# Kernel tuning notes

Measured on AMD Instinct MI355X. Metric: run time of the kernel, lower is better.

Reference implementation:

```python
import jax, jax.numpy as jnp
import numpy as np

DIM = 128
GROUPS = [1, 2, 2, 3]


def setup_inputs() -> dict:
    key = jax.random.key(0)
    ks = jax.random.split(key, 8)
    c = DIM
    def p(k, shape, scale=0.02):
        return jax.random.normal(k, shape, dtype=jnp.float32) * scale
    return {
        "x": jax.random.normal(ks[0], (8, c, 128, 128), dtype=jnp.float32),
        "temperature": jnp.ones((4, 1, 1), dtype=jnp.float32),
        "w_qkv": p(ks[1], (3 * c, c)),            # Conv2d(dim, 3*dim, 1), bias=False
        "w_dw": p(ks[2], (3 * c, 1, 3, 3)),        # depthwise 3x3, groups=3*dim
        "w_proj": p(ks[3], (c, c)),                # Conv2d(dim, dim, 1), bias=False
        "w_gate": p(ks[4], (c, c)),                # Intra gatingConv (Conv1d k=1)
        "b_gate": jnp.zeros((c,), jnp.float32),
        "w_down": p(ks[5], (c // 2, c)),           # Intra down
        "b_down": jnp.zeros((c // 2,), jnp.float32),
        "w_up": p(ks[6], (c, c // 2)),             # Intra up
        "b_up": jnp.zeros((c,), jnp.float32),
    }


def _group_sizes(c):
    total = sum(GROUPS)
    sizes = [int(r / total * c) for r in GROUPS]
    sizes[-1] += c - sum(sizes)
    return sizes


def _forward(x, temperature, w_qkv, w_dw, w_proj, w_gate, b_gate,
             w_down, b_down, w_up, b_up):
    b, c, h, w = x.shape
    L = h * w
    # qkv = dwconv3x3(conv1x1(x))
    qkv = jnp.einsum('bchw,oc->bohw', x, w_qkv)
    qkv = jax.lax.conv_general_dilated(
        qkv, w_dw, (1, 1), 'SAME', feature_group_count=3 * c,
        dimension_numbers=('NCHW', 'OIHW', 'NCHW'))
    q, k, v = jnp.split(qkv.reshape(b, 3 * c, L), 3, axis=1)
    # ReGroup: sort channels by mean q activation (descending), split into groups
    channel_mean = q.mean(axis=(0, 2))            # (c,)
    idx = jnp.argsort(-channel_mean)
    q, k, v = q[:, idx], k[:, idx], v[:, idx]
    sizes = _group_sizes(c)
    outs, caches, cache_means = [], [], []
    start = 0
    for i, g in enumerate(sizes):
        qg = q[:, start:start + g]
        kg = k[:, start:start + g]
        vg = v[:, start:start + g]
        start += g
        qn = qg / jnp.maximum(jnp.linalg.norm(qg, axis=-1, keepdims=True), 1e-12)
        kn = kg / jnp.maximum(jnp.linalg.norm(kg, axis=-1, keepdims=True), 1e-12)
        attn = jax.nn.softmax(
            jnp.einsum('bcl,bdl->bcd', qn, kn) * temperature[i, 0, 0], axis=-1)
        outs.append(jnp.einsum('bcd,bdl->bcl', attn, vg))   # (b, g, L)
        tc = jax.lax.stop_gradient(qn + kn)                 # detached cache
        caches.append(tc)
        # per-group mean over L, channel-tiled/padded to c (for cache update)
        gm = tc.mean(axis=-1)                               # (b, g)
        rep = max(1, c // g)
        gm = jnp.tile(gm, (1, rep))
        gm = gm[:, :c] if gm.shape[1] >= c else jnp.pad(gm, ((0, 0), (0, c - gm.shape[1])))
        cache_means.append(gm)
    out_all = jnp.concatenate(outs, axis=1)       # (b, c, L)
    tmp_caches = jnp.concatenate(caches, axis=1)  # (b, c, L)
    # CalculateCurrentLayerCache: bilinear upsample of (1,1) map == broadcast
    s = int(L ** 0.5 + 0.9999)
    acc = sum(cache_means) / float(len(cache_means))        # (b, c)
    qv_cache = jnp.broadcast_to((acc * 0.9)[:, :, None, None], (b, c, s, s))
    # Intra cache modulation: gated = gelu(conv(x1+x2)) * (x1+x2); up(down(gated))
    sxy = out_all + tmp_caches
    gating = jax.nn.gelu(jnp.einsum('bcl,oc->bol', sxy, w_gate) + b_gate[:, None],
                         approximate=False)
    gated = gating * sxy
    mod = jnp.einsum('bcl,oc->bol', gated, w_down) + b_down[:, None]
    mod = jnp.einsum('bcl,oc->bol', mod, w_up) + b_up[:, None]
    out_all = mod + out_all
    out_all = jnp.einsum('bchw,oc->bohw', out_all.reshape(b, c, h, w), w_proj)
    return out_all, qv_cache


def reference(x, temperature, w_qkv, w_dw, w_proj, w_gate, b_gate,
              w_down, b_down, w_up, b_up):
    return _forward(x, temperature, w_qkv, w_dw, w_proj, w_gate, b_gate,
                    w_down, b_down, w_up, b_up)
```

## Files before the change

### kernel.cpp

```cpp
#include <hip/hip_runtime.h>
#include <math.h>

#define B_ 8
#define C_ 128
#define O3_ 384
#define H_ 128
#define W_ 128
#define L_ 16384
#define NS_ 64
#define MAXP_ 2304

typedef float f32x4 __attribute__((ext_vector_type(4)));
typedef short bf16x8 __attribute__((ext_vector_type(8)));

static __device__ __forceinline__ ushort f2bf(float f) {
    uint u = __float_as_uint(f);
    u += 0x7fffu + ((u >> 16) & 1u);
    return (ushort)(u >> 16);
}
static __device__ __forceinline__ float bf2f(ushort h) {
    return __uint_as_float(((uint)h) << 16);
}

__global__ __launch_bounds__(256) void wsplit_k(
    const float* __restrict__ wa, const float* __restrict__ wb,
    const float* __restrict__ wc, const float* __restrict__ wd,
    short* __restrict__ ha, short* __restrict__ la,
    short* __restrict__ hb, short* __restrict__ lb,
    short* __restrict__ hc, short* __restrict__ lc,
    short* __restrict__ hd, short* __restrict__ ld)
{
    const int sel = blockIdx.y;
    const float* w = sel == 0 ? wa : (sel == 1 ? wb : (sel == 2 ? wc : wd));
    short* ph = sel == 0 ? ha : (sel == 1 ? hb : (sel == 2 ? hc : hd));
    short* pl = sel == 0 ? la : (sel == 1 ? lb : (sel == 2 ? lc : ld));
    const int n = sel == 0 ? 49152 : (sel == 1 ? 16384 : 8192);
    const int i = blockIdx.x * 256 + threadIdx.x;
    if (i < n) {
        float v = w[i];
        ushort h = f2bf(v);
        ph[i] = (short)h;
        pl[i] = (short)f2bf(v - bf2f(h));
    }
}

__global__ __launch_bounds__(256) void wsplit1_k(const float* __restrict__ w,
    short* __restrict__ ph, short* __restrict__ pl, int n)
{
    const int i = blockIdx.x * 256 + threadIdx.x;
    if (i < n) {
        float v = w[i];
        ushort h = f2bf(v);
        ph[i] = (short)h;
        pl[i] = (short)f2bf(v - bf2f(h));
    }
}

__global__ __launch_bounds__(256) void transp_k(const float* __restrict__ x,
    short* __restrict__ xhi, short* __restrict__ xlo)
{
    __shared__ float t[128][33];
    const int b = blockIdx.y;
    const int l0 = blockIdx.x * 32;
    const int tid = threadIdx.x;
    {
        const int c = tid >> 1, half = tid & 1;
        const float* src = x + ((size_t)b * C_ + c) * L_ + l0 + half * 16;
#pragma unroll
        for (int u = 0; u < 4; u++) {
            float4 v = *reinterpret_cast<const float4*>(src + u * 4);
            t[c][half * 16 + u * 4 + 0] = v.x;
            t[c][half * 16 + u * 4 + 1] = v.y;
            t[c][half * 16 + u * 4 + 2] = v.z;
            t[c][half * 16 + u * 4 + 3] = v.w;
        }
    }
    __syncthreads();
    {
        const int l = tid >> 3, strip = tid & 7;
        uint hi[8], lo[8];
#pragma unroll
        for (int i = 0; i < 8; i++) {
            float a0 = t[strip * 16 + 2 * i][l], a1 = t[strip * 16 + 2 * i + 1][l];
            ushort h0 = f2bf(a0), h1 = f2bf(a1);
            ushort g0 = f2bf(a0 - bf2f(h0)), g1 = f2bf(a1 - bf2f(h1));
            hi[i] = (uint)h0 | ((uint)h1 << 16);
            lo[i] = (uint)g0 | ((uint)g1 << 16);
        }
        size_t ob = ((size_t)b * L_ + l0 + l) * C_ + strip * 16;
        uint4* ph = reinterpret_cast<uint4*>(xhi + ob);
        uint4* pl = reinterpret_cast<uint4*>(xlo + ob);
        ph[0] = *reinterpret_cast<uint4*>(&hi[0]);
        ph[1] = *reinterpret_cast<uint4*>(&hi[4]);
        pl[0] = *reinterpret_cast<uint4*>(&lo[0]);
        pl[1] = *reinterpret_cast<uint4*>(&lo[4]);
    }
}

template<int KD, int OT, int MODE>
__global__ __launch_bounds__(256) void mgemm_k(
    const short* __restrict__ Whi, const short* __restrict__ Wlo,
    const float* __restrict__ bias,
    const short* __restrict__ Ahi, const short* __restrict__ Alo,
    const float* __restrict__ E0,
    float* __restrict__ Yf, short* __restrict__ Yhi, short* __restrict__ Ylo)
{
    constexpr int NR = OT / 32;
    constexpr int T = KD / 32;
    constexpr int BPT = (OT * 4) / 256;
    __shared__ short sAh[128][40];
    __shared__ short sAl[128][40];
    __shared__ short sBh[OT][40];
    __shared__ short sBl[OT][40];
    const int tid = threadIdx.x;
    const int lane = tid & 63;
    const int wid = tid >> 6;
    const int wr = wid >> 1, wc = wid & 1;
    const int oB = blockIdx.x * OT;
    const int lB = blockIdx.y * 128;
    const int ON = gridDim.x * OT;
    const int b = blockIdx.z;
    const int ln15 = lane & 15, lg = lane >> 4;

    const int al0 = tid >> 2, ac8 = (tid & 3) * 8;
    const size_t abase = ((size_t)b * L_ + lB + al0) * KD + ac8;

    f32x4 acc[4][NR];
#pragma unroll
    for (int m = 0; m < 4; m++)
#pragma unroll
        for (int n = 0; n < NR; n++)
#pragma unroll
            for (int r = 0; r < 4; r++) acc[m][n][r] = 0.f;

    bf16x8 pAh[2], pAl[2], pBh[BPT], pBl[BPT];

    auto ldA = [&](int t) {
#pragma unroll
        for (int p = 0; p < 2; p++) {
            size_t g = abase + (size_t)p * 64 * KD + t * 32;
            pAh[p] = *reinterpret_cast<const bf16x8*>(Ahi + g);
            pAl[p] = *reinterpret_cast<const bf16x8*>(Alo + g);
        }
    };
    auto ldB = [&](int t) {
#pragma unroll
        for (int p = 0; p < BPT; p++) {
            int idx = tid + p * 256;
            int o = idx >> 2, c8 = (idx & 3) * 8;
            size_t g = (size_t)(oB + o) * KD + t * 32 + c8;
            pBh[p] = *reinterpret_cast<const bf16x8*>(Whi + g);
            pBl[p] = *reinterpret_cast<const bf16x8*>(Wlo + g);
        }
    };
    auto stAB = [&]() {
#pragma unroll
        for (int p = 0; p < 2; p++) {
            *reinterpret_cast<bf16x8*>(&sAh[al0 + p * 64][ac8]) = pAh[p];
            *reinterpret_cast<bf16x8*>(&sAl[al0 + p * 64][ac8]) = pAl[p];
        }
#pragma unroll
        for (int p = 0; p < BPT; p++) {
            int idx = tid + p * 256;
            int o = idx >> 2, c8 = (idx & 3) * 8;
            *reinterpret_cast<bf16x8*>(&sBh[o][c8]) = pBh[p];
            *reinterpret_cast<bf16x8*>(&sBl[o][c8]) = pBl[p];
        }
    };

    ldA(0); ldB(0);
    stAB();
    __syncthreads();

    for (int t = 0; t < T; t++) {
        if (t + 1 < T) { ldA(t + 1); ldB(t + 1); }
        bf16x8 Ah[4], Al[4];
#pragma unroll
        for (int m = 0; m < 4; m++) {
            int row = wr * 64 + m * 16 + ln15;
            Ah[m] = *reinterpret_cast<const bf16x8*>(&sAh[row][lg * 8]);
            Al[m] = *reinterpret_cast<const bf16x8*>(&sAl[row][lg * 8]);
        }
#pragma unroll
        for (int n = 0; n < NR; n++) {
            int brow = wc * (OT / 2) + n * 16 + ln15;
            bf16x8 Bh = *reinterpret_cast<const bf16x8*>(&sBh[brow][lg * 8]);
            bf16x8 Bl = *reinterpret_cast<const bf16x8*>(&sBl[brow][lg * 8]);
#pragma unroll
            for (int m = 0; m < 4; m++) {
                acc[m][n] = __builtin_amdgcn_mfma_f32_16x16x32_bf16(Ah[m], Bh, acc[m][n], 0, 0, 0);
                acc[m][n] = __builtin_amdgcn_mfma_f32_16x16x32_bf16(Ah[m], Bl, acc[m][n], 0, 0, 0);
                acc[m][n] = __builtin_amdgcn_mfma_f32_16x16x32_bf16(Al[m], Bh, acc[m][n], 0, 0, 0);
            }
        }
        __syncthreads();
        if (t + 1 < T) { stAB(); __syncthreads(); }
    }

#pragma unroll
    for (int m = 0; m < 4; m++) {
        const int lg4 = lB + wr * 64 + m * 16 + lg * 4;
#pragma unroll
        for (int n = 0; n < NR; n++) {
            const int o = oB + wc * (OT / 2) + n * 16 + ln15;
            if constexpr (MODE == 4) {
                float4 r4 = {acc[m][n][0], acc[m][n][1], acc[m][n][2], acc[m][n][3]};
                *reinterpret_cast<float4*>(&Yf[((size_t)b * ON + o) * L_ + lg4]) = r4;
            } else {
                float bv = bias[o];
#pragma unroll
                for (int r = 0; r < 4; r++) {
                    size_t yi = ((size_t)b * L_ + lg4 + r) * ON + o;
                    float a = acc[m][n][r] + bv;
                    if constexpr (MODE == 1) {
                        float sxy = bf2f((ushort)Ahi[yi]) + bf2f((ushort)Alo[yi]);
                        a = 0.5f * a * (1.f + erff(a * 0.70710678118654752f)) * sxy;
                    }
                    if constexpr (MODE == 3) a += E0[yi];
                    ushort h = f2bf(a);
                    ushort g = f2bf(a - bf2f(h));
                    Yhi[yi] = (short)h;
                    Ylo[yi] = (short)g;
                }
            }
        }
    }
}

__global__ __launch_bounds__(256) void dwconv_k(const float* __restrict__ in,
    const float* __restrict__ wdw, float* __restrict__ outp,
    float* __restrict__ sumq, float* __restrict__ sumk,
    float* __restrict__ ssq, float* __restrict__ ssk)
{
    const int ch = blockIdx.x, b = blockIdx.y;
    const int tid = threadIdx.x;
    const int tx = tid & 31, band = tid >> 5;
    const int x0 = tx * 4;
    const int y0 = band * 16;
    const size_t base = ((size_t)b * O3_ + ch) * L_;
    const float* wp = wdw + ch * 9;
    float w0 = wp[0], w1 = wp[1], w2 = wp[2], w3 = wp[3], w4 = wp[4],
          w5 = wp[5], w6 = wp[6], w7 = wp[7], w8 = wp[8];

    float s1 = 0.f, s2 = 0.f;
    float b0[6], b1[6], b2[6];

    auto loadrow = [&](int gy, float* r) {
        if ((unsigned)gy < (unsigned)H_) {
            const float* rp = in + base + (size_t)gy * W_;
            float4 m = *reinterpret_cast<const float4*>(rp + x0);
            r[0] = (x0 > 0) ? rp[x0 - 1] : 0.f;
            r[1] = m.x; r[2] = m.y; r[3] = m.z; r[4] = m.w;
            r[5] = (x0 < W_ - 4) ? rp[x0 + 4] : 0.f;
        } else {
            r[0] = r[1] = r[2] = r[3] = r[4] = r[5] = 0.f;
        }
    };
    auto conv3 = [&](const float* ra, const float* rb, const float* rc, int yy) {
        float o0 = ra[0]*w0 + ra[1]*w1 + ra[2]*w2 + rb[0]*w3 + rb[1]*w4 + rb[2]*w5 + rc[0]*w6 + rc[1]*w7 + rc[2]*w8;
        float o1 = ra[1]*w0 + ra[2]*w1 + ra[3]*w2 + rb[1]*w3 + rb[2]*w4 + rb[3]*w5 + rc[1]*w6 + rc[2]*w7 + rc[3]*w8;
        float o2 = ra[2]*w0 + ra[3]*w1 + ra[4]*w2 + rb[2]*w3 + rb[3]*w4 + rb[4]*w5 + rc[2]*w6 + rc[3]*w7 + rc[4]*w8;
        float o3 = ra[3]*w0 + ra[4]*w1 + ra[5]*w2 + rb[3]*w3 + rb[4]*w4 + rb[5]*w5 + rc[3]*w6 + rc[4]*w7 + rc[5]*w8;
        float4 o4 = {o0, o1, o2, o3};
        *reinterpret_cast<float4*>(&outp[base + (size_t)(y0 + yy) * W_ + x0]) = o4;
        s1 += (o0 + o1) + (o2 + o3);
        s2 += o0*o0 + o1*o1 + o2*o2 + o3*o3;
    };

    loadrow(y0 - 1, b0);
    loadrow(y0,     b1);
#pragma unroll
    for (int y3 = 0; y3 < 15; y3 += 3) {
        loadrow(y0 + y3 + 1, b2); conv3(b0, b1, b2, y3);
        loadrow(y0 + y3 + 2, b0); conv3(b1, b2, b0, y3 + 1);
        loadrow(y0 + y3 + 3, b1); conv3(b2, b0, b1, y3 + 2);
    }
    loadrow(y0 + 16, b2); conv3(b0, b1, b2, 15);

    __shared__ float r1[256], r2[256];
    if (ch < 256) {
        r1[tid] = s1; r2[tid] = s2;
        __syncthreads();
        for (int st = 128; st > 0; st >>= 1) {
            if (tid < st) { r1[tid] += r1[tid + st]; r2[tid] += r2[tid + st]; }
            __syncthreads();
        }
        if (tid == 0) {
            if (ch < 128) { sumq[b * 128 + ch] = r1[0]; ssq[b * 128 + ch] = r2[0]; }
            else          { sumk[b * 128 + ch - 128] = r1[0]; ssk[b * 128 + ch - 128] = r2[0]; }
        }
    }
}

__global__ void combine_k(const float* __restrict__ sumq, const float* __restrict__ sumk,
    const float* __restrict__ ssq, const float* __restrict__ ssk,
    int* __restrict__ idxp, float* __restrict__ rqc, float* __restrict__ rkc,
    float* __restrict__ gm)
{
    const int t = threadIdx.x;
    __shared__ double cms[128];
    double s = 0.0;
    for (int b = 0; b < B_; b++) s += (double)sumq[b * 128 + t];
    cms[t] = s;
    float rqv[B_], rkv[B_];
    for (int b = 0; b < B_; b++) {
        rqv[b] = 1.f / fmaxf(sqrtf(ssq[b * 128 + t]), 1e-12f);
        rkv[b] = 1.f / fmaxf(sqrtf(ssk[b * 128 + t]), 1e-12f);
        rqc[b * 128 + t] = rqv[b];
        rkc[b * 128 + t] = rkv[b];
    }
    __syncthreads();
    const double mv = cms[t];
    int r = 0;
    for (int j = 0; j < 128; j++) {
        double o = cms[j];
        if (o > mv || (o == mv && j < t)) r++;
    }
    idxp[r] = t;
    for (int b = 0; b < B_; b++)
        gm[b * 128 + r] = (rqv[b] * sumq[b * 128 + t] + rkv[b] * sumk[b * 128 + t]) * (1.0f / L_);
}

template<int G>
__global__ __launch_bounds__(256) void score_k(const float* __restrict__ dw, const int* __restrict__ idxp,
    int start, int gi, float* __restrict__ spart)
{
    constexpr int TS = G / 16;
    const int split = blockIdx.x, b = blockIdx.y;
    const int tid = threadIdx.x, tx = tid & 15, ty = tid >> 4;
    __shared__ float sQ[G][66];
    __shared__ float sK[G][66];
    __shared__ int sc[G];
    if (tid < G) sc[tid] = idxp[start + tid];
    __syncthreads();

    float acc[TS][TS];
#pragma unroll
    for (int i = 0; i < TS; i++)
#pragma unroll
        for (int j = 0; j < TS; j++) acc[i][j] = 0.f;

    const int l0 = split * (L_ / NS_);
    constexpr int LPT = (G * 64) / 256;
    for (int chk = 0; chk < L_ / NS_; chk += 64) {
#pragma unroll
        for (int i = 0; i < LPT; i++) {
            int id = tid + i * 256;
            int row = id >> 6, lc = id & 63;
            size_t base = ((size_t)b * O3_ + sc[row]) * L_ + l0 + chk + lc;
            sQ[row][lc] = dw[base];
            sK[row][lc] = dw[base + (size_t)128 * L_];
        }
        __syncthreads();
#pragma unroll
        for (int kk = 0; kk < 64; kk++) {
            float qv[TS], kv[TS];
#pragma unroll
            for (int j = 0; j < TS; j++) { qv[j] = sQ[ty * TS + j][kk]; kv[j] = sK[tx * TS + j][kk]; }
#pragma unroll
            for (int i = 0; i < TS; i++)
#pragma unroll
                for (int j = 0; j < TS; j++)
                    acc[i][j] = fmaf(qv[i], kv[j], acc[i][j]);
        }
        __syncthreads();
    }
    float* op = spart + (((size_t)(b * 4 + gi)) * NS_ + split) * MAXP_;
#pragma unroll
    for (int i = 0; i < TS; i++)
#pragma unroll
        for (int j = 0; j < TS; j++)
            op[(ty * TS + i) * G + tx * TS + j] = acc[i][j];
}

__global__ __launch_bounds__(256) void softmax_k(const float* __restrict__ spart,
    const float* __restrict__ rqc, const float* __restrict__ rkc, const int* __restrict__ idxp,
    const float* __restrict__ temp, float* __restrict__ attn)
{
    const int gi = blockIdx.x, b = blockIdx.y;
    const int g = (gi == 0) ? 16 : (gi == 3 ? 48 : 32);
    const int start = (gi == 0) ? 0 : (gi == 1 ? 16 : (gi == 2 ? 48 : 80));
    __shared__ float S[MAXP_];
    __shared__ int sidx[48];
    if (threadIdx.x < g) sidx[threadIdx.x] = idxp[start + threadIdx.x];
    __syncthreads();
    const float tv = temp[gi];
    for (int p = threadIdx.x; p < g * g; p += 256) {
        float s = 0.f;
        const float* sp = spart + ((size_t)(b * 4 + gi)) * NS_ * MAXP_ + p;
        for (int k = 0; k < NS_; k++) s += sp[(size_t)k * MAXP_];
        int cc = p / g, dd = p - cc * g;
        S[p] = s * rqc[b * 128 + sidx[cc]] * rkc[b * 128 + sidx[dd]] * tv;
    }
    __syncthreads();
    const int wv = threadIdx.x >> 6, lane = threadIdx.x & 63;
    for (int r = wv; r < g; r += 4) {
        float val = (lane < g) ? S[r * g + lane] : -1e30f;
        float mx = val;
        for (int m = 32; m > 0; m >>= 1) mx = fmaxf(mx, __shfl_xor(mx, m));
        float e = (lane < g) ? expf(val - mx) : 0.f;
        float sum = e;
        for (int m = 32; m > 0; m >>= 1) sum += __shfl_xor(sum, m);
        if (lane < g) attn[((size_t)(b * 4 + gi)) * MAXP_ + r * g + lane] = e / sum;
    }
}

template<int G>
__global__ __launch_bounds__(256) void av3_k(const float* __restrict__ dw, const int* __restrict__ idxp,
    const float* __restrict__ rqc, const float* __restrict__ rkc,
    const float* __restrict__ attn, int start, int gi,
    float* __restrict__ outallT, short* __restrict__ sxyhi, short* __restrict__ sxylo)
{
    constexpr int C4 = G / 4;
    constexpr int GP = G + 1;
    const int b = blockIdx.y;
    const int lB = blockIdx.x * 64;
    const int tid = threadIdx.x;
    __shared__ float sA[G * GP];
    __shared__ float sV[64][GP];
    __shared__ int cv[G];
    __shared__ float rqs[G], rks[G];
    if (tid < G) {
        int c0 = idxp[start + tid];
        cv[tid] = c0;
        rqs[tid] = rqc[b * 128 + c0];
        rks[tid] = rkc[b * 128 + c0];
    }
    for (int p = tid; p < G * G; p += 256) {
        int cc = p / G, dd = p - cc * G;
        sA[cc * GP + dd] = attn[((size_t)(b * 4 + gi)) * MAXP_ + p];
    }
    __syncthreads();
    for (int idx = tid; idx < 64 * G; idx += 256) {
        int l = idx & 63, d = idx >> 6;
        sV[l][d] = dw[((size_t)b * O3_ + 256 + cv[d]) * L_ + lB + l];
    }
    __syncthreads();
    const int strip = tid & 3, l = tid >> 2;
    float acc[C4];
#pragma unroll
    for (int j = 0; j < C4; j++) acc[j] = 0.f;
    for (int d = 0; d < G; d++) {
        float vd = sV[l][d];
#pragma unroll
        for (int j = 0; j < C4; j++)
            acc[j] = fmaf(sA[(strip * C4 + j) * GP + d], vd, acc[j]);
    }
    const size_t ob = ((size_t)b * L_ + lB + l) * C_ + start + strip * C4;
    float sv[C4];
#pragma unroll
    for (int j = 0; j < C4; j++) {
        int c = strip * C4 + j;
        float q = dw[((size_t)b * O3_ + cv[c]) * L_ + lB + l];
        float k = dw[((size_t)b * O3_ + 128 + cv[c]) * L_ + lB + l];
        sv[j] = acc[j] + rqs[c] * q + rks[c] * k;
    }
#pragma unroll
    for (int j = 0; j < C4; j += 4) {
        float4 o4 = {acc[j], acc[j + 1], acc[j + 2], acc[j + 3]};
        *reinterpret_cast<float4*>(&outallT[ob + j]) = o4;
    }
#pragma unroll
    for (int j = 0; j < C4; j += 2) {
        ushort h0 = f2bf(sv[j]), h1 = f2bf(sv[j + 1]);
        ushort g0 = f2bf(sv[j] - bf2f(h0)), g1 = f2bf(sv[j + 1] - bf2f(h1));
        *reinterpret_cast<uint*>(&sxyhi[ob + j]) = (uint)h0 | ((uint)h1 << 16);
        *reinterpret_cast<uint*>(&sxylo[ob + j]) = (uint)g0 | ((uint)g1 << 16);
    }
}

__global__ __launch_bounds__(256) void qvc_k(const float* __restrict__ gm, float* __restrict__ outq)
{
    const int cpos = blockIdx.x, b = blockIdx.y;
    const float* g = gm + b * 128;
    float v = g[cpos & 15] + g[16 + (cpos & 31)] + g[48 + (cpos & 31)];
    if (cpos < 96) v += g[80 + (cpos % 48)];
    v *= 0.225f;
    float4 vv = {v, v, v, v};
    float4* op = reinterpret_cast<float4*>(outq + ((size_t)b * C_ + cpos) * L_);
    for (int i = threadIdx.x; i < L_ / 4; i += 256) op[i] = vv;
}

extern "C" void kernel_launch(void* const* d_in, const int* in_sizes, int n_in,
                              void* d_out, int out_size, void* d_ws, size_t ws_size,
                              hipStream_t stream)
{
    const float* x     = (const float*)d_in[0];
    const float* temp  = (const float*)d_in[1];
    const float* wqkv  = (const float*)d_in[2];
    const float* wdw   = (const float*)d_in[3];
    const float* wproj = (const float*)d_in[4];
    const float* wgate = (const float*)d_in[5];
    const float* bgate = (const float*)d_in[6];
    const float* wdown = (const float*)d_in[7];
    const float* bdown = (const float*)d_in[8];
    const float* wup   = (const float*)d_in[9];
    const float* bup   = (const float*)d_in[10];
    float* out = (float*)d_out;
    float* ws  = (float*)d_ws;

    float* qkvCL = ws;
    float* dwCL  = ws + 50331648ull;
    short* xThi  = (short*)(ws + 50331648ull);
    short* xTlo  = xThi + 16777216ull;
    float* outallT = ws;
    short* sxyhi   = (short*)(ws + 16777216ull);
    short* sxylo   = sxyhi + 16777216ull;
    short* gatedhi = (short*)(ws + 33554432ull);
    short* gatedlo = gatedhi + 16777216ull;
    short* mod1hi  = (short*)(ws + 16777216ull);
    short* mod1lo  = mod1hi + 8388608ull;
    short* out2hi  = (short*)(ws + 33554432ull);
    short* out2lo  = out2hi + 16777216ull;
    short* wprojh  = (short*)(ws + 25165824ull);
    short* wprojl  = wprojh + 16384ull;

    float* spart = out;
    float* attn  = out + 4718592ull;
    float* sumq  = out + 4800000ull;
    float* sumk  = out + 4801024ull;
    float* ssq   = out + 4802048ull;
    float* ssk   = out + 4803072ull;
    float* rqc   = out + 4804096ull;
    float* rkc   = out + 4805120ull;
    float* gm    = out + 4806144ull;
    int*   idxp  = (int*)(out + 4807168ull);
    short* wqkvh = (short*)(out + 4900000ull);
    short* wqkvl = (short*)(out + 4924576ull);
    short* wgateh= (short*)(out + 4949152ull);
    short* wgatel= (short*)(out + 4957344ull);
    short* wdownh= (short*)(out + 4965536ull);
    short* wdownl= (short*)(out + 4969632ull);
    short* wuph  = (short*)(out + 4973728ull);
    short* wupl  = (short*)(out + 4977824ull);

    wsplit_k<<<dim3(192, 4), 256, 0, stream>>>(wqkv, wgate, wdown, wup,
        wqkvh, wqkvl, wgateh, wgatel, wdownh, wdownl, wuph, wupl);
    transp_k<<<dim3(512, 8), 256, 0, stream>>>(x, xThi, xTlo);
    mgemm_k<128, 128, 4><<<dim3(3, 128, 8), 256, 0, stream>>>(
        wqkvh, wqkvl, nullptr, xThi, xTlo, nullptr, qkvCL, nullptr, nullptr);
    dwconv_k<<<dim3(384, 8), 256, 0, stream>>>(qkvCL, wdw, dwCL, sumq, sumk, ssq, ssk);
    combine_k<<<1, 128, 0, stream>>>(sumq, sumk, ssq, ssk, idxp, rqc, rkc, gm);
    score_k<16><<<dim3(NS_, 8), 256, 0, stream>>>(dwCL, idxp, 0, 0, spart);
    score_k<32><<<dim3(NS_, 8), 256, 0, stream>>>(dwCL, idxp, 16, 1, spart);
    score_k<32><<<dim3(NS_, 8), 256, 0, stream>>>(dwCL, idxp, 48, 2, spart);
    score_k<48><<<dim3(NS_, 8), 256, 0, stream>>>(dwCL, idxp, 80, 3, spart);
    softmax_k<<<dim3(4, 8), 256, 0, stream>>>(spart, rqc, rkc, idxp, temp, attn);
    av3_k<16><<<dim3(256, 8), 256, 0, stream>>>(dwCL, idxp, rqc, rkc, attn, 0, 0, outallT, sxyhi, sxylo);
    av3_k<32><<<dim3(256, 8), 256, 0, stream>>>(dwCL, idxp, rqc, rkc, attn, 16, 1, outallT, sxyhi, sxylo);
    av3_k<32><<<dim3(256, 8), 256, 0, stream>>>(dwCL, idxp, rqc, rkc, attn, 48, 2, outallT, sxyhi, sxylo);
    av3_k<48><<<dim3(256, 8), 256, 0, stream>>>(dwCL, idxp, rqc, rkc, attn, 80, 3, outallT, sxyhi, sxylo);
    mgemm_k<128, 128, 1><<<dim3(1, 128, 8), 256, 0, stream>>>(
        wgateh, wgatel, bgate, sxyhi, sxylo, nullptr, nullptr, gatedhi, gatedlo);
    qvc_k<<<dim3(128, 8), 256, 0, stream>>>(gm, out + 16777216ull);
    mgemm_k<128, 64, 2><<<dim3(1, 128, 8), 256, 0, stream>>>(
        wdownh, wdownl, bdown, gatedhi, gatedlo, nullptr, nullptr, mod1hi, mod1lo);
    mgemm_k<64, 128, 3><<<dim3(1, 128, 8), 256, 0, stream>>>(
        wuph, wupl, bup, mod1hi, mod1lo, outallT, nullptr, out2hi, out2lo);
    wsplit1_k<<<64, 256, 0, stream>>>(wproj, wprojh, wprojl, 16384);
    mgemm_k<128, 128, 4><<<dim3(1, 128, 8), 256, 0, stream>>>(
        wprojh, wprojl, nullptr, out2hi, out2lo, nullptr, out, nullptr, nullptr);
}
```

Baseline: 729.6 us.

## Drop LDS staging in split-bf16 GEMM and use warp shuffles for dwconv halos

The MFMA GEMM kernel no longer stages A and B tiles through shared memory. Each wave now loads its 64-row A fragments directly from global memory with double buffering in registers, and reads weight fragments straight from global memory (expected to hit cache). Block shapes are re-parameterized so one block covers all output channels, which removes the syncthreads barriers and the LDS round trip. The depthwise conv gets its left and right halo pixels through warp shuffles instead of extra scalar global loads. The cost is more global and L2 traffic for the weights and higher register pressure.

```diff
diff --git a/kernel.cpp b/kernel.cpp
--- a/kernel.cpp
+++ b/kernel.cpp
@@ -97,95 +97,51 @@
     }
 }
 
-template<int KD, int OT, int MODE>
-__global__ __launch_bounds__(256) void mgemm_k(
+template<int KD, int ON, int MODE, int LW>
+__global__ __launch_bounds__(LW*(ON/64)*64) void mgemm_k(
     const short* __restrict__ Whi, const short* __restrict__ Wlo,
     const float* __restrict__ bias,
     const short* __restrict__ Ahi, const short* __restrict__ Alo,
     const float* __restrict__ E0,
     float* __restrict__ Yf, short* __restrict__ Yhi, short* __restrict__ Ylo)
 {
-    constexpr int NR = OT / 32;
+    constexpr int WO = ON / 64;
     constexpr int T = KD / 32;
-    constexpr int BPT = (OT * 4) / 256;
-    __shared__ short sAh[128][40];
-    __shared__ short sAl[128][40];
-    __shared__ short sBh[OT][40];
-    __shared__ short sBl[OT][40];
     const int tid = threadIdx.x;
     const int lane = tid & 63;
     const int wid = tid >> 6;
-    const int wr = wid >> 1, wc = wid & 1;
-    const int oB = blockIdx.x * OT;
-    const int lB = blockIdx.y * 128;
-    const int ON = gridDim.x * OT;
-    const int b = blockIdx.z;
+    const int wr = wid / WO, wc = wid % WO;
+    const int b = blockIdx.y;
+    const int lB = blockIdx.x * (LW * 64) + wr * 64;
     const int ln15 = lane & 15, lg = lane >> 4;
 
-    const int al0 = tid >> 2, ac8 = (tid & 3) * 8;
-    const size_t abase = ((size_t)b * L_ + lB + al0) * KD + ac8;
-
-    f32x4 acc[4][NR];
+    const size_t arow0 = ((size_t)b * L_ + lB + ln15) * KD + lg * 8;
+    const size_t brow0 = (size_t)(wc * 64 + ln15) * KD + lg * 8;
+
+    f32x4 acc[4][4];
 #pragma unroll
     for (int m = 0; m < 4; m++)
 #pragma unroll
-        for (int n = 0; n < NR; n++)
+        for (int n = 0; n < 4; n++)
 #pragma unroll
             for (int r = 0; r < 4; r++) acc[m][n][r] = 0.f;
 
-    bf16x8 pAh[2], pAl[2], pBh[BPT], pBl[BPT];
-
-    auto ldA = [&](int t) {
-#pragma unroll
-        for (int p = 0; p < 2; p++) {
-            size_t g = abase + (size_t)p * 64 * KD + t * 32;
-            pAh[p] = *reinterpret_cast<const bf16x8*>(Ahi + g);
-            pAl[p] = *reinterpret_cast<const bf16x8*>(Alo + g);
+    bf16x8 A0h[4], A0l[4], A1h[4], A1l[4];
+
+    auto ldA = [&](bf16x8* Ah, bf16x8* Al, int t) {
+#pragma unroll
+        for (int m = 0; m < 4; m++) {
+            size_t g = arow0 + (size_t)(m * 16) * KD + t * 32;
+            Ah[m] = *reinterpret_cast<const bf16x8*>(Ahi + g);
+            Al[m] = *reinterpret_cast<const bf16x8*>(Alo + g);
         }
     };
-    auto ldB = [&](int t) {
-#pragma unroll
-        for (int p = 0; p < BPT; p++) {
-            int idx = tid + p * 256;
-            int o = idx >> 2, c8 = (idx & 3) * 8;
-            size_t g = (size_t)(oB + o) * KD + t * 32 + c8;
-            pBh[p] = *reinterpret_cast<const bf16x8*>(Whi + g);
-            pBl[p] = *reinterpret_cast<const bf16x8*>(Wlo + g);
-        }
-    };
-    auto stAB = [&]() {
-#pragma unroll
-        for (int p = 0; p < 2; p++) {
-            *reinterpret_cast<bf16x8*>(&sAh[al0 + p * 64][ac8]) = pAh[p];
-            *reinterpret_cast<bf16x8*>(&sAl[al0 + p * 64][ac8]) = pAl[p];
-        }
-#pragma unroll
-        for (int p = 0; p < BPT; p++) {
-            int idx = tid + p * 256;
-            int o = idx >> 2, c8 = (idx & 3) * 8;
-            *reinterpret_cast<bf16x8*>(&sBh[o][c8]) = pBh[p];
-            *reinterpret_cast<bf16x8*>(&sBl[o][c8]) = pBl[p];
-        }
-    };
-
-    ldA(0); ldB(0);
-    stAB();
-    __syncthreads();
-
-    for (int t = 0; t < T; t++) {
-        if (t + 1 < T) { ldA(t + 1); ldB(t + 1); }
-        bf16x8 Ah[4], Al[4];
-#pragma unroll
-        for (int m = 0; m < 4; m++) {
-            int row = wr * 64 + m * 16 + ln15;
-            Ah[m] = *reinterpret_cast<const bf16x8*>(&sAh[row][lg * 8]);
-            Al[m] = *reinterpret_cast<const bf16x8*>(&sAl[row][lg * 8]);
-        }
-#pragma unroll
-        for (int n = 0; n < NR; n++) {
-            int brow = wc * (OT / 2) + n * 16 + ln15;
-            bf16x8 Bh = *reinterpret_cast<const bf16x8*>(&sBh[brow][lg * 8]);
-            bf16x8 Bl = *reinterpret_cast<const bf16x8*>(&sBl[brow][lg * 8]);
+    auto comp = [&](const bf16x8* Ah, const bf16x8* Al, int t) {
+#pragma unroll
+        for (int n = 0; n < 4; n++) {
+            size_t g = brow0 + (size_t)(n * 16) * KD + t * 32;
+            bf16x8 Bh = *reinterpret_cast<const bf16x8*>(Whi + g);
+            bf16x8 Bl = *reinterpret_cast<const bf16x8*>(Wlo + g);
 #pragma unroll
             for (int m = 0; m < 4; m++) {
                 acc[m][n] = __builtin_amdgcn_mfma_f32_16x16x32_bf16(Ah[m], Bh, acc[m][n], 0, 0, 0);
@@ -193,24 +149,31 @@
                 acc[m][n] = __builtin_amdgcn_mfma_f32_16x16x32_bf16(Al[m], Bh, acc[m][n], 0, 0, 0);
             }
         }
-        __syncthreads();
-        if (t + 1 < T) { stAB(); __syncthreads(); }
+    };
+
+    ldA(A0h, A0l, 0);
+#pragma unroll
+    for (int t = 0; t < T; t += 2) {
+        if (t + 1 < T) ldA(A1h, A1l, t + 1);
+        comp(A0h, A0l, t);
+        if (t + 2 < T) ldA(A0h, A0l, t + 2);
+        comp(A1h, A1l, t + 1);
     }
 
 #pragma unroll
     for (int m = 0; m < 4; m++) {
-        const int lg4 = lB + wr * 64 + m * 16 + lg * 4;
-#pragma unroll
-        for (int n = 0; n < NR; n++) {
-            const int o = oB + wc * (OT / 2) + n * 16 + ln15;
+        const int l = lB + m * 16 + lg * 4;
+#pragma unroll
+        for (int n = 0; n < 4; n++) {
+            const int o = wc * 64 + n * 16 + ln15;
             if constexpr (MODE == 4) {
                 float4 r4 = {acc[m][n][0], acc[m][n][1], acc[m][n][2], acc[m][n][3]};
-                *reinterpret_cast<float4*>(&Yf[((size_t)b * ON + o) * L_ + lg4]) = r4;
+                *reinterpret_cast<float4*>(&Yf[((size_t)b * ON + o) * L_ + l]) = r4;
             } else {
                 float bv = bias[o];
 #pragma unroll
                 for (int r = 0; r < 4; r++) {
-                    size_t yi = ((size_t)b * L_ + lg4 + r) * ON + o;
+                    size_t yi = ((size_t)b * L_ + l + r) * ON + o;
                     float a = acc[m][n][r] + bv;
                     if constexpr (MODE == 1) {
                         float sxy = bf2f((ushort)Ahi[yi]) + bf2f((ushort)Alo[yi]);
@@ -246,15 +209,14 @@
     float b0[6], b1[6], b2[6];
 
     auto loadrow = [&](int gy, float* r) {
-        if ((unsigned)gy < (unsigned)H_) {
-            const float* rp = in + base + (size_t)gy * W_;
-            float4 m = *reinterpret_cast<const float4*>(rp + x0);
-            r[0] = (x0 > 0) ? rp[x0 - 1] : 0.f;
-            r[1] = m.x; r[2] = m.y; r[3] = m.z; r[4] = m.w;
-            r[5] = (x0 < W_ - 4) ? rp[x0 + 4] : 0.f;
-        } else {
-            r[0] = r[1] = r[2] = r[3] = r[4] = r[5] = 0.f;
-        }
+        float4 m = {0.f, 0.f, 0.f, 0.f};
+        if ((unsigned)gy < (unsigned)H_)
+            m = *reinterpret_cast<const float4*>(in + base + (size_t)gy * W_ + x0);
+        float left  = __shfl_up(m.w, 1, 32);
+        float right = __shfl_down(m.x, 1, 32);
+        r[0] = (tx == 0) ? 0.f : left;
+        r[1] = m.x; r[2] = m.y; r[3] = m.z; r[4] = m.w;
+        r[5] = (tx == 31) ? 0.f : right;
     };
     auto conv3 = [&](const float* ra, const float* rb, const float* rc, int yy) {
         float o0 = ra[0]*w0 + ra[1]*w1 + ra[2]*w2 + rb[0]*w3 + rb[1]*w4 + rb[2]*w5 + rc[0]*w6 + rc[1]*w7 + rc[2]*w8;
@@ -537,7 +499,7 @@
     wsplit_k<<<dim3(192, 4), 256, 0, stream>>>(wqkv, wgate, wdown, wup,
         wqkvh, wqkvl, wgateh, wgatel, wdownh, wdownl, wuph, wupl);
     transp_k<<<dim3(512, 8), 256, 0, stream>>>(x, xThi, xTlo);
-    mgemm_k<128, 128, 4><<<dim3(3, 128, 8), 256, 0, stream>>>(
+    mgemm_k<128, 384, 4, 1><<<dim3(256, 8), 384, 0, stream>>>(
         wqkvh, wqkvl, nullptr, xThi, xTlo, nullptr, qkvCL, nullptr, nullptr);
     dwconv_k<<<dim3(384, 8), 256, 0, stream>>>(qkvCL, wdw, dwCL, sumq, sumk, ssq, ssk);
     combine_k<<<1, 128, 0, stream>>>(sumq, sumk, ssq, ssk, idxp, rqc, rkc, gm);
@@ -550,14 +512,14 @@
     av3_k<32><<<dim3(256, 8), 256, 0, stream>>>(dwCL, idxp, rqc, rkc, attn, 16, 1, outallT, sxyhi, sxylo);
     av3_k<32><<<dim3(256, 8), 256, 0, stream>>>(dwCL, idxp, rqc, rkc, attn, 48, 2, outallT, sxyhi, sxylo);
     av3_k<48><<<dim3(256, 8), 256, 0, stream>>>(dwCL, idxp, rqc, rkc, attn, 80, 3, outallT, sxyhi, sxylo);
-    mgemm_k<128, 128, 1><<<dim3(1, 128, 8), 256, 0, stream>>>(
+    mgemm_k<128, 128, 1, 2><<<dim3(128, 8), 256, 0, stream>>>(
         wgateh, wgatel, bgate, sxyhi, sxylo, nullptr, nullptr, gatedhi, gatedlo);
     qvc_k<<<dim3(128, 8), 256, 0, stream>>>(gm, out + 16777216ull);
-    mgemm_k<128, 64, 2><<<dim3(1, 128, 8), 256, 0, stream>>>(
+    mgemm_k<128, 64, 2, 4><<<dim3(64, 8), 256, 0, stream>>>(
         wdownh, wdownl, bdown, gatedhi, gatedlo, nullptr, nullptr, mod1hi, mod1lo);
-    mgemm_k<64, 128, 3><<<dim3(1, 128, 8), 256, 0, stream>>>(
+    mgemm_k<64, 128, 3, 2><<<dim3(128, 8), 256, 0, stream>>>(
         wuph, wupl, bup, mod1hi, mod1lo, outallT, nullptr, out2hi, out2lo);
     wsplit1_k<<<64, 256, 0, stream>>>(wproj, wprojh, wprojl, 16384);
-    mgemm_k<128, 128, 4><<<dim3(1, 128, 8), 256, 0, stream>>>(
+    mgemm_k<128, 128, 4, 2><<<dim3(128, 8), 256, 0, stream>>>(
         wprojh, wprojl, nullptr, out2hi, out2lo, nullptr, out, nullptr, nullptr);
 }
```

New measurement: 778.1 us. +6.6%, slower.

## Keep whole weight tile resident in swizzled LDS and re-tile MFMA GEMM warps

Applied to the files above, without the earlier changes.

The split-bf16 MFMA GEMM now loads the full weight slice (all K) into shared memory once per block, using an XOR-swizzled layout, instead of restaging B every K step. Only the activation tile is streamed, also swizzled to avoid bank conflicts. Warp layout is derived from the output tile width, so the 64-wide down-projection covers 256 rows per block, and its grid is halved to match. The aim is less global and LDS traffic and fewer bank conflicts, at the cost of more shared memory per block, which may lower occupancy.

```diff
diff --git a/kernel.cpp b/kernel.cpp
--- a/kernel.cpp
+++ b/kernel.cpp
@@ -105,112 +105,125 @@
     const float* __restrict__ E0,
     float* __restrict__ Yf, short* __restrict__ Yhi, short* __restrict__ Ylo)
 {
-    constexpr int NR = OT / 32;
-    constexpr int T = KD / 32;
-    constexpr int BPT = (OT * 4) / 256;
-    __shared__ short sAh[128][40];
-    __shared__ short sAl[128][40];
-    __shared__ short sBh[OT][40];
-    __shared__ short sBl[OT][40];
+    constexpr int WC = OT / 64;
+    constexpr int WR = 4 / WC;
+    constexpr int LT = WR * 64;
+    constexpr int T  = KD / 32;
+    constexpr int ABYTES = LT * 64;
+    constexpr int BBYTES = OT * KD * 2;
+    constexpr int CA = WR;
+    constexpr int CB = (OT * KD) / 2048;
+    __shared__ __align__(16) char sAh[ABYTES];
+    __shared__ __align__(16) char sAl[ABYTES];
+    __shared__ __align__(16) char sBh[BBYTES];
+    __shared__ __align__(16) char sBl[BBYTES];
+
     const int tid = threadIdx.x;
     const int lane = tid & 63;
     const int wid = tid >> 6;
-    const int wr = wid >> 1, wc = wid & 1;
+    const int wr = wid / WC, wc = wid % WC;
     const int oB = blockIdx.x * OT;
-    const int lB = blockIdx.y * 128;
+    const int lB = blockIdx.y * LT;
     const int ON = gridDim.x * OT;
-    const int b = blockIdx.z;
+    const int b  = blockIdx.z;
     const int ln15 = lane & 15, lg = lane >> 4;
-
-    const int al0 = tid >> 2, ac8 = (tid & 3) * 8;
-    const size_t abase = ((size_t)b * L_ + lB + al0) * KD + ac8;
-
-    f32x4 acc[4][NR];
+    const int m0A = (ln15 >> 1) & 3;
+    const int m0B = ln15 & 3;
+    const int m1B = (ln15 >> 2) & (T - 1);
+
+    const size_t abase = ((size_t)b * L_ + lB) * KD;
+
+    {
+#pragma unroll
+        for (int p = 0; p < CB; p++) {
+            const int id = tid + p * 256;
+            const int row = id / (KD / 8), cs = id % (KD / 8);
+            const int tt = cs >> 2, ks = cs & 3;
+            const size_t src = (size_t)(oB + row) * KD + cs * 8;
+            const int dst = row * (KD * 2) + ((tt ^ ((row >> 2) & (T - 1))) * 64)
+                          + ((ks ^ (row & 3)) << 4);
+            *reinterpret_cast<uint4*>(sBh + dst) = *reinterpret_cast<const uint4*>(Whi + src);
+            *reinterpret_cast<uint4*>(sBl + dst) = *reinterpret_cast<const uint4*>(Wlo + src);
+        }
+    }
+
+    uint4 pAh[CA], pAl[CA];
+    auto ldgA = [&](int t) {
+#pragma unroll
+        for (int p = 0; p < CA; p++) {
+            const int id = tid + p * 256;
+            const int row = id >> 2, s = id & 3;
+            const size_t src = abase + (size_t)row * KD + t * 32 + s * 8;
+            pAh[p] = *reinterpret_cast<const uint4*>(Ahi + src);
+            pAl[p] = *reinterpret_cast<const uint4*>(Alo + src);
+        }
+    };
+    auto stA = [&]() {
+#pragma unroll
+        for (int p = 0; p < CA; p++) {
+            const int id = tid + p * 256;
+            const int row = id >> 2, s = id & 3;
+            const int dst = row * 64 + ((s ^ ((row >> 1) & 3)) << 4);
+            *reinterpret_cast<uint4*>(sAh + dst) = pAh[p];
+            *reinterpret_cast<uint4*>(sAl + dst) = pAl[p];
+        }
+    };
+
+    f32x4 acc[4][4];
 #pragma unroll
     for (int m = 0; m < 4; m++)
 #pragma unroll
-        for (int n = 0; n < NR; n++)
+        for (int n = 0; n < 4; n++)
 #pragma unroll
             for (int r = 0; r < 4; r++) acc[m][n][r] = 0.f;
 
-    bf16x8 pAh[2], pAl[2], pBh[BPT], pBl[BPT];
-
-    auto ldA = [&](int t) {
-#pragma unroll
-        for (int p = 0; p < 2; p++) {
-            size_t g = abase + (size_t)p * 64 * KD + t * 32;
-            pAh[p] = *reinterpret_cast<const bf16x8*>(Ahi + g);
-            pAl[p] = *reinterpret_cast<const bf16x8*>(Alo + g);
-        }
-    };
-    auto ldB = [&](int t) {
-#pragma unroll
-        for (int p = 0; p < BPT; p++) {
-            int idx = tid + p * 256;
-            int o = idx >> 2, c8 = (idx & 3) * 8;
-            size_t g = (size_t)(oB + o) * KD + t * 32 + c8;
-            pBh[p] = *reinterpret_cast<const bf16x8*>(Whi + g);
-            pBl[p] = *reinterpret_cast<const bf16x8*>(Wlo + g);
-        }
-    };
-    auto stAB = [&]() {
-#pragma unroll
-        for (int p = 0; p < 2; p++) {
-            *reinterpret_cast<bf16x8*>(&sAh[al0 + p * 64][ac8]) = pAh[p];
-            *reinterpret_cast<bf16x8*>(&sAl[al0 + p * 64][ac8]) = pAl[p];
-        }
-#pragma unroll
-        for (int p = 0; p < BPT; p++) {
-            int idx = tid + p * 256;
-            int o = idx >> 2, c8 = (idx & 3) * 8;
-            *reinterpret_cast<bf16x8*>(&sBh[o][c8]) = pBh[p];
-            *reinterpret_cast<bf16x8*>(&sBl[o][c8]) = pBl[p];
-        }
-    };
-
-    ldA(0); ldB(0);
-    stAB();
+    ldgA(0);
+    stA();
     __syncthreads();
 
     for (int t = 0; t < T; t++) {
-        if (t + 1 < T) { ldA(t + 1); ldB(t + 1); }
-        bf16x8 Ah[4], Al[4];
+        bf16x8 Ah[4], Al[4], Bh[4], Bl[4];
 #pragma unroll
         for (int m = 0; m < 4; m++) {
-            int row = wr * 64 + m * 16 + ln15;
-            Ah[m] = *reinterpret_cast<const bf16x8*>(&sAh[row][lg * 8]);
-            Al[m] = *reinterpret_cast<const bf16x8*>(&sAl[row][lg * 8]);
-        }
-#pragma unroll
-        for (int n = 0; n < NR; n++) {
-            int brow = wc * (OT / 2) + n * 16 + ln15;
-            bf16x8 Bh = *reinterpret_cast<const bf16x8*>(&sBh[brow][lg * 8]);
-            bf16x8 Bl = *reinterpret_cast<const bf16x8*>(&sBl[brow][lg * 8]);
+            const int row = wr * 64 + m * 16 + ln15;
+            const int ab = row * 64 + ((lg ^ m0A) << 4);
+            Ah[m] = *reinterpret_cast<const bf16x8*>(sAh + ab);
+            Al[m] = *reinterpret_cast<const bf16x8*>(sAl + ab);
+        }
+#pragma unroll
+        for (int n = 0; n < 4; n++) {
+            const int row = wc * 64 + n * 16 + ln15;
+            const int bb = row * (KD * 2) + ((t ^ m1B) * 64) + ((lg ^ m0B) << 4);
+            Bh[n] = *reinterpret_cast<const bf16x8*>(sBh + bb);
+            Bl[n] = *reinterpret_cast<const bf16x8*>(sBl + bb);
+        }
+        __syncthreads();
+        if (t + 1 < T) ldgA(t + 1);
+#pragma unroll
+        for (int n = 0; n < 4; n++)
 #pragma unroll
             for (int m = 0; m < 4; m++) {
-                acc[m][n] = __builtin_amdgcn_mfma_f32_16x16x32_bf16(Ah[m], Bh, acc[m][n], 0, 0, 0);
-                acc[m][n] = __builtin_amdgcn_mfma_f32_16x16x32_bf16(Ah[m], Bl, acc[m][n], 0, 0, 0);
-                acc[m][n] = __builtin_amdgcn_mfma_f32_16x16x32_bf16(Al[m], Bh, acc[m][n], 0, 0, 0);
+                acc[m][n] = __builtin_amdgcn_mfma_f32_16x16x32_bf16(Ah[m], Bh[n], acc[m][n], 0, 0, 0);
+                acc[m][n] = __builtin_amdgcn_mfma_f32_16x16x32_bf16(Ah[m], Bl[n], acc[m][n], 0, 0, 0);
+                acc[m][n] = __builtin_amdgcn_mfma_f32_16x16x32_bf16(Al[m], Bh[n], acc[m][n], 0, 0, 0);
             }
-        }
-        __syncthreads();
-        if (t + 1 < T) { stAB(); __syncthreads(); }
+        if (t + 1 < T) { stA(); __syncthreads(); }
     }
 
 #pragma unroll
     for (int m = 0; m < 4; m++) {
-        const int lg4 = lB + wr * 64 + m * 16 + lg * 4;
-#pragma unroll
-        for (int n = 0; n < NR; n++) {
-            const int o = oB + wc * (OT / 2) + n * 16 + ln15;
+        const int l = lB + wr * 64 + m * 16 + lg * 4;
+#pragma unroll
+        for (int n = 0; n < 4; n++) {
+            const int o = oB + wc * 64 + n * 16 + ln15;
             if constexpr (MODE == 4) {
                 float4 r4 = {acc[m][n][0], acc[m][n][1], acc[m][n][2], acc[m][n][3]};
-                *reinterpret_cast<float4*>(&Yf[((size_t)b * ON + o) * L_ + lg4]) = r4;
+                *reinterpret_cast<float4*>(&Yf[((size_t)b * ON + o) * L_ + l]) = r4;
             } else {
                 float bv = bias[o];
 #pragma unroll
                 for (int r = 0; r < 4; r++) {
-                    size_t yi = ((size_t)b * L_ + lg4 + r) * ON + o;
+                    size_t yi = ((size_t)b * L_ + l + r) * ON + o;
                     float a = acc[m][n][r] + bv;
                     if constexpr (MODE == 1) {
                         float sxy = bf2f((ushort)Ahi[yi]) + bf2f((ushort)Alo[yi]);
@@ -553,7 +566,7 @@
     mgemm_k<128, 128, 1><<<dim3(1, 128, 8), 256, 0, stream>>>(
         wgateh, wgatel, bgate, sxyhi, sxylo, nullptr, nullptr, gatedhi, gatedlo);
     qvc_k<<<dim3(128, 8), 256, 0, stream>>>(gm, out + 16777216ull);
-    mgemm_k<128, 64, 2><<<dim3(1, 128, 8), 256, 0, stream>>>(
+    mgemm_k<128, 64, 2><<<dim3(1, 64, 8), 256, 0, stream>>>(
         wdownh, wdownl, bdown, gatedhi, gatedlo, nullptr, nullptr, mod1hi, mod1lo);
     mgemm_k<64, 128, 3><<<dim3(1, 128, 8), 256, 0, stream>>>(
         wuph, wupl, bup, mod1hi, mod1lo, outallT, nullptr, out2hi, out2lo);
```

New measurement: 766.2 us. 1.05x slower.
